# Kernel tuning notes

Measured on AMD Instinct MI355X. Metric: run time of the kernel, lower is better.

The kernel has to match this reference:

```python
import jax, jax.numpy as jnp
import numpy as np
from jax import lax

CHANNEL_N = 16
ALPHA_CHANNEL = 3
FIRE_RATE = 0.5


def get_sobel(size):
    # generalized Sobel: g(x,y) = x / (x^2 + y^2), zero at center
    s = size // 2
    yy, xx = np.mgrid[-s:s + 1, -s:s + 1].astype(np.float32)
    denom = xx * xx + yy * yy
    denom[s, s] = 1.0
    gx = xx / denom
    gy = yy / denom
    gx /= np.sum(np.abs(gx))
    gy /= np.sum(np.abs(gy))
    return gx, gy


def build_kernel(C):
    # stack the six sobel stencils (sizes 3/5/7), zero-padded to 7x7 so a single
    # SAME depthwise conv reproduces the three separate padded convs exactly
    ks = []
    for size in (3, 5, 7):
        gx, gy = get_sobel(size)
        p = (7 - size) // 2
        ks.append(np.pad(gx, p))
        ks.append(np.pad(gy, p))
    k = np.stack(ks, 0)                # [6,7,7]
    k = np.tile(k, (C, 1, 1))          # [6C,7,7], channel-major groups
    return jnp.asarray(k.transpose(1, 2, 0)[:, :, None, :])  # HWIO [7,7,1,6C]


def _maxpool(x, size):
    p = size // 2
    return lax.reduce_window(x, -jnp.inf, lax.max, (1, size, size, 1), (1, 1, 1, 1),
                             [(0, 0), (p, p), (p, p), (0, 0)])


def _life_mask(x):
    alpha = x[..., ALPHA_CHANNEL:ALPHA_CHANNEL + 1]
    return _maxpool(alpha, 3) > 0.1


def _update(x, stoch_u, valid_mask, kern, W0, b0, W1):
    N, H, W, C = x.shape
    pre_life = _life_mask(x)
    y = lax.conv_general_dilated(x, kern, (1, 1), [(3, 3), (3, 3)],
                                 dimension_numbers=("NHWC", "HWIO", "NHWC"),
                                 feature_group_count=C)  # [N,H,W,6C] channel-major
    # reorder to (y1 all C, y2 all C, ...) matching torch.cat order
    y = y.reshape(N, H, W, C, 6).transpose(0, 1, 2, 4, 3).reshape(N, H, W, 6 * C)
    perc = jnp.concatenate([x, y, _maxpool(x, 5)], axis=-1)  # [N,H,W,8C]
    h = jax.nn.relu(perc @ W0 + b0)  # [N,H,W,256]
    dx = h @ W1                      # [N,H,W,C]
    dx = dx * (stoch_u > FIRE_RATE).astype(x.dtype)
    x = x + dx
    life = (pre_life & _life_mask(x)).astype(x.dtype)
    return x * life * valid_mask


def setup_inputs():
    key = jax.random.key(0)
    k1, k2, k3, k4 = jax.random.split(key, 4)
    B, H, W, C, steps = 8, 256, 256, CHANNEL_N, 16
    x = jax.random.uniform(k1, (B, H, W, C), jnp.float32)
    valid_mask = jnp.ones((B, H, W, 1), jnp.float32)
    stoch = jax.random.uniform(k2, (steps, B, H, W, 1), jnp.float32)
    W0 = jax.random.normal(k3, (8 * C, 256), jnp.float32) * 0.05
    b0 = jnp.zeros((256,), jnp.float32)
    W1 = jax.random.normal(k4, (256, C), jnp.float32) * 0.02
    return {"x": x, "valid_mask": valid_mask, "stoch": stoch,
            "W0": W0, "b0": b0, "W1": W1, "steps": steps}


def reference(x, valid_mask, stoch, W0, b0, W1, steps):
    kern = build_kernel(x.shape[-1])

    def step(carry, su):
        return _update(carry, su, valid_mask, kern, W0, b0, W1), None

    x, _ = lax.scan(step, x, stoch[:steps])
    return x
```

## Files before the change

### kernel.cpp

```cpp
#include <hip/hip_runtime.h>
#include <math.h>


#define HW 256
#define NPIX (8*HW*HW)

typedef __attribute__((ext_vector_type(8))) short short8;
typedef __attribute__((ext_vector_type(4))) float f32x4;

__device__ __forceinline__ float4 f4max(float4 a, float4 b) {
    return make_float4(fmaxf(a.x,b.x), fmaxf(a.y,b.y), fmaxf(a.z,b.z), fmaxf(a.w,b.w));
}
__device__ __forceinline__ unsigned short bf16_rne(float v) {
    unsigned int u = __float_as_uint(v);
    unsigned int r = u + 0x7FFFu + ((u >> 16) & 1u);
    return (unsigned short)(r >> 16);
}
__device__ __forceinline__ float bf16f(unsigned short h) {
    return __uint_as_float(((unsigned int)h) << 16);
}

__global__ void init_kernel(const float* __restrict__ W0,
                            const float* __restrict__ W1,
                            float* __restrict__ filt,
                            unsigned short* __restrict__ W0hiT,
                            unsigned short* __restrict__ W0loT,
                            unsigned short* __restrict__ W1hiT2,
                            unsigned short* __restrict__ W1loT2) {
    int t = blockIdx.x * blockDim.x + threadIdx.x;
    int nth = gridDim.x * blockDim.x;
    for (int idx = t; idx < 32768; idx += nth) {
        int j = idx >> 7, k = idx & 127;
        float v = W0[k * 256 + j];
        unsigned short hi = bf16_rne(v);
        unsigned short lo = bf16_rne(v - bf16f(hi));
        W0hiT[idx] = hi;
        W0loT[idx] = lo;
    }
    for (int idx = t; idx < 4096; idx += nth) {
        int ch = idx >> 8, j = idx & 255;
        float v = W1[j * 16 + ch];
        unsigned short hi = bf16_rne(v);
        unsigned short lo = bf16_rne(v - bf16f(hi));
        W1hiT2[idx] = hi;
        W1loT2[idx] = lo;
    }
    if (t < 6) {
        int f = t;
        int size = 3 + 2*(f >> 1);
        int p0 = (7 - size) >> 1;
        int isY = f & 1;
        float vals[49];
        float norm = 0.f;
        for (int a = 0; a < 7; a++) {
            for (int b = 0; b < 7; b++) {
                float v = 0.f;
                if (a >= p0 && a < p0+size && b >= p0 && b < p0+size) {
                    float fy = (float)(a - 3), fx = (float)(b - 3);
                    float den = fx*fx + fy*fy;
                    if (den == 0.f) den = 1.f;
                    v = (isY ? fy : fx) / den;
                }
                vals[a*7+b] = v;
                norm += fabsf(v);
            }
        }
        float inv = 1.f / norm;
        for (int i = 0; i < 49; i++) filt[f*49 + i] = vals[i] * inv;
    }
}

__launch_bounds__(256, 2)
__global__ void step_main(const float* __restrict__ x,
                          float* __restrict__ xmid,
                          const unsigned char* __restrict__ prelife_in,
                          unsigned char* __restrict__ prelife_out,
                          const float* __restrict__ filt_g,
                          const unsigned short* __restrict__ W0hiT,
                          const unsigned short* __restrict__ W0loT,
                          const unsigned short* __restrict__ W1hiT2,
                          const unsigned short* __restrict__ W1loT2,
                          const float* __restrict__ b0,
                          const float* __restrict__ stoch_s,
                          const float* __restrict__ valid,
                          int apply_mask) {
    __shared__ float smem[19712];
    float*          xs      = smem;
    float*          filt_s  = smem + 3920;
    unsigned short* w0hA    = (unsigned short*)smem;
    unsigned short* w0lA    = (unsigned short*)(smem + 2176);
    unsigned short* w0hB    = (unsigned short*)(smem + 4352);
    unsigned short* w0lB    = (unsigned short*)(smem + 6528);
    unsigned short* perc_hi = (unsigned short*)(smem + 8704);
    unsigned short* perc_lo = (unsigned short*)(smem + 13056);
    unsigned short* hbuf_hi = (unsigned short*)(smem + 17408);
    unsigned short* hbuf_lo = (unsigned short*)(smem + 18560);

    const int t   = threadIdx.x;
    const int b   = blockIdx.z;
    const int ty0 = blockIdx.y * 8;
    const int tx0 = blockIdx.x * 8;

    const int sgbase = ((t >> 3) << 7) + ((t & 7) << 4);
    const int swds   = (t >> 3) * 136 + ((t & 7) << 4);
    uint4 sh0 = *(const uint4*)&W0hiT[sgbase];
    uint4 sh1 = *(const uint4*)&W0hiT[sgbase + 8];
    uint4 sl0 = *(const uint4*)&W0loT[sgbase];
    uint4 sl1 = *(const uint4*)&W0loT[sgbase + 8];

    for (int i = t; i < 294; i += 256) filt_s[i] = filt_g[i];

    if (t < 196) {
        const int ly = t / 14, lx = t - ly*14;
        const int gy = ty0 + ly - 3, gx = tx0 + lx - 3;
        const bool inb = ((unsigned)gy < 256u) && ((unsigned)gx < 256u);
        float4 v0 = make_float4(0.f,0.f,0.f,0.f), v1 = v0, v2 = v0, v3 = v0;
        if (inb) {
            const int pix = (b << 16) + (gy << 8) + gx;
            const float* srcp = &x[(size_t)pix << 4];
            v0 = *(const float4*)(srcp);
            v1 = *(const float4*)(srcp + 4);
            v2 = *(const float4*)(srcp + 8);
            v3 = *(const float4*)(srcp + 12);
            if (apply_mask) {
                float m = -INFINITY;
                #pragma unroll
                for (int dy = -1; dy <= 1; dy++) {
                    #pragma unroll
                    for (int dxo = -1; dxo <= 1; dxo++) {
                        int yy = gy + dy, xx2 = gx + dxo;
                        if ((unsigned)yy < 256u && (unsigned)xx2 < 256u)
                            m = fmaxf(m, x[((size_t)((b<<16)+(yy<<8)+xx2) << 4) + 3]);
                    }
                }
                float s = (prelife_in[pix] != 0 && m > 0.1f) ? valid[pix] : 0.f;
                v0.x *= s; v0.y *= s; v0.z *= s; v0.w *= s;
                v1.x *= s; v1.y *= s; v1.z *= s; v1.w *= s;
                v2.x *= s; v2.y *= s; v2.z *= s; v2.w *= s;
                v3.x *= s; v3.y *= s; v3.z *= s; v3.w *= s;
            }
        }
        float* dstp = &xs[t * 20];
        *(float4*)(dstp)      = v0;
        *(float4*)(dstp + 4)  = v1;
        *(float4*)(dstp + 8)  = v2;
        *(float4*)(dstp + 12) = v3;
    }
    __syncthreads();

    {
        const int p  = t & 63;
        const int q  = t >> 6;
        const int py = p >> 3, px1 = p & 7;
        const int gy = ty0 + py, gx = tx0 + px1;
        const int q4 = q << 2;

        float4 y4[6];
        #pragma unroll
        for (int f = 0; f < 6; f++) y4[f] = make_float4(0.f,0.f,0.f,0.f);

        #pragma unroll
        for (int a = 0; a < 7; a++) {
            #pragma unroll
            for (int bb = 0; bb < 7; bb++) {
                float4 xv = *(const float4*)&xs[((py+a)*14 + (px1+bb))*20 + q4];
                {
                    float w4 = filt_s[4*49 + a*7 + bb];
                    float w5 = filt_s[5*49 + a*7 + bb];
                    y4[4].x = fmaf(w4, xv.x, y4[4].x); y4[4].y = fmaf(w4, xv.y, y4[4].y);
                    y4[4].z = fmaf(w4, xv.z, y4[4].z); y4[4].w = fmaf(w4, xv.w, y4[4].w);
                    y4[5].x = fmaf(w5, xv.x, y4[5].x); y4[5].y = fmaf(w5, xv.y, y4[5].y);
                    y4[5].z = fmaf(w5, xv.z, y4[5].z); y4[5].w = fmaf(w5, xv.w, y4[5].w);
                }
                if (a >= 1 && a <= 5 && bb >= 1 && bb <= 5) {
                    float w2 = filt_s[2*49 + a*7 + bb];
                    float w3 = filt_s[3*49 + a*7 + bb];
                    y4[2].x = fmaf(w2, xv.x, y4[2].x); y4[2].y = fmaf(w2, xv.y, y4[2].y);
                    y4[2].z = fmaf(w2, xv.z, y4[2].z); y4[2].w = fmaf(w2, xv.w, y4[2].w);
                    y4[3].x = fmaf(w3, xv.x, y4[3].x); y4[3].y = fmaf(w3, xv.y, y4[3].y);
                    y4[3].z = fmaf(w3, xv.z, y4[3].z); y4[3].w = fmaf(w3, xv.w, y4[3].w);
                }
                if (a >= 2 && a <= 4 && bb >= 2 && bb <= 4) {
                    float w0 = filt_s[0*49 + a*7 + bb];
                    float w1 = filt_s[1*49 + a*7 + bb];
                    y4[0].x = fmaf(w0, xv.x, y4[0].x); y4[0].y = fmaf(w0, xv.y, y4[0].y);
                    y4[0].z = fmaf(w0, xv.z, y4[0].z); y4[0].w = fmaf(w0, xv.w, y4[0].w);
                    y4[1].x = fmaf(w1, xv.x, y4[1].x); y4[1].y = fmaf(w1, xv.y, y4[1].y);
                    y4[1].z = fmaf(w1, xv.z, y4[1].z); y4[1].w = fmaf(w1, xv.w, y4[1].w);
                }
            }
        }
        float4 m5 = make_float4(-INFINITY,-INFINITY,-INFINITY,-INFINITY);
        #pragma unroll
        for (int dy = -2; dy <= 2; dy++) {
            #pragma unroll
            for (int dx2 = -2; dx2 <= 2; dx2++) {
                if ((unsigned)(gy+dy) < 256u && (unsigned)(gx+dx2) < 256u)
                    m5 = f4max(m5, *(const float4*)&xs[((py+3+dy)*14 + (px1+3+dx2))*20 + q4]);
            }
        }
        float4 xc = *(const float4*)&xs[((py+3)*14 + (px1+3))*20 + q4];

        #define SPLIT4(arridx, v) { \
            unsigned short h0 = bf16_rne((v).x), h1 = bf16_rne((v).y); \
            unsigned short h2 = bf16_rne((v).z), h3 = bf16_rne((v).w); \
            unsigned short l0 = bf16_rne((v).x - bf16f(h0)); \
            unsigned short l1 = bf16_rne((v).y - bf16f(h1)); \
            unsigned short l2 = bf16_rne((v).z - bf16f(h2)); \
            unsigned short l3 = bf16_rne((v).w - bf16f(h3)); \
            *(ushort4*)&perc_hi[arridx] = make_ushort4(h0,h1,h2,h3); \
            *(ushort4*)&perc_lo[arridx] = make_ushort4(l0,l1,l2,l3); }

        const int prow = p * 136;
        SPLIT4(prow +       q4, xc);
        SPLIT4(prow + 16  + q4, y4[0]);
        SPLIT4(prow + 32  + q4, y4[1]);
        SPLIT4(prow + 48  + q4, y4[2]);
        SPLIT4(prow + 64  + q4, y4[3]);
        SPLIT4(prow + 80  + q4, y4[4]);
        SPLIT4(prow + 96  + q4, y4[5]);
        SPLIT4(prow + 112 + q4, m5);
        #undef SPLIT4

        if (q == 0) {
            float pre = -INFINITY;
            #pragma unroll
            for (int dy = -1; dy <= 1; dy++) {
                #pragma unroll
                for (int dx2 = -1; dx2 <= 1; dx2++) {
                    if ((unsigned)(gy+dy) < 256u && (unsigned)(gx+dx2) < 256u)
                        pre = fmaxf(pre, xs[((py+3+dy)*14 + (px1+3+dx2))*20 + 3]);
                }
            }
            prelife_out[(b << 16) + (gy << 8) + gx] = (pre > 0.1f) ? 1 : 0;
        }
    }
    __syncthreads();

    const int lane = t & 63;
    const int wid  = t >> 6;
    const int l15  = lane & 15;
    const int l4   = lane >> 4;
    const int aoff  = (wid*16 + l15)*136 + 8*l4;
    const int boff0 = (l15)*136 + 8*l4;
    const int boff1 = (16 + l15)*136 + 8*l4;
    const int hwr   = (wid*16 + 4*l4)*36 + l15;
    const int hrd   = (wid*16 + l15)*36 + 8*l4;
    const int w1off = l15*256 + 8*l4;

    short8 ah0 = *(const short8*)&perc_hi[aoff +  0];
    short8 ah1 = *(const short8*)&perc_hi[aoff + 32];
    short8 ah2 = *(const short8*)&perc_hi[aoff + 64];
    short8 ah3 = *(const short8*)&perc_hi[aoff + 96];
    short8 al0 = *(const short8*)&perc_lo[aoff +  0];
    short8 al1 = *(const short8*)&perc_lo[aoff + 32];
    short8 al2 = *(const short8*)&perc_lo[aoff + 64];
    short8 al3 = *(const short8*)&perc_lo[aoff + 96];

    f32x4 dacc = {0.f, 0.f, 0.f, 0.f};

    *(uint4*)&w0hA[swds]     = sh0;
    *(uint4*)&w0hA[swds + 8] = sh1;
    *(uint4*)&w0lA[swds]     = sl0;
    *(uint4*)&w0lA[swds + 8] = sl1;
    sh0 = *(const uint4*)&W0hiT[sgbase + 4096];
    sh1 = *(const uint4*)&W0hiT[sgbase + 4096 + 8];
    sl0 = *(const uint4*)&W0loT[sgbase + 4096];
    sl1 = *(const uint4*)&W0loT[sgbase + 4096 + 8];
    __syncthreads();

    #pragma unroll 1
    for (int jc = 0; jc < 8; jc++) {
        const unsigned short* wrdh = (jc & 1) ? w0hB : w0hA;
        const unsigned short* wrdl = (jc & 1) ? w0lB : w0lA;
        unsigned short*       wwrh = (jc & 1) ? w0hA : w0hB;
        unsigned short*       wwrl = (jc & 1) ? w0lA : w0lB;

        f32x4 acc0 = {0.f, 0.f, 0.f, 0.f};
        f32x4 acc1 = {0.f, 0.f, 0.f, 0.f};

        #define KSTEP(accv, boff, AH, AL, ks) { \
            short8 bh = *(const short8*)&wrdh[(boff) + (ks)*32]; \
            short8 bl = *(const short8*)&wrdl[(boff) + (ks)*32]; \
            accv = __builtin_amdgcn_mfma_f32_16x16x32_bf16(AL, bh, accv, 0, 0, 0); \
            accv = __builtin_amdgcn_mfma_f32_16x16x32_bf16(AH, bl, accv, 0, 0, 0); \
            accv = __builtin_amdgcn_mfma_f32_16x16x32_bf16(AH, bh, accv, 0, 0, 0); }

        KSTEP(acc0, boff0, ah0, al0, 0)
        KSTEP(acc0, boff0, ah1, al1, 1)
        KSTEP(acc0, boff0, ah2, al2, 2)
        KSTEP(acc0, boff0, ah3, al3, 3)
        KSTEP(acc1, boff1, ah0, al0, 0)
        KSTEP(acc1, boff1, ah1, al1, 1)
        KSTEP(acc1, boff1, ah2, al2, 2)
        KSTEP(acc1, boff1, ah3, al3, 3)
        #undef KSTEP

        {
            float bias0 = b0[jc*32 + l15];
            float bias1 = b0[jc*32 + 16 + l15];
            #pragma unroll
            for (int r = 0; r < 4; r++) {
                float h0 = fmaxf(acc0[r] + bias0, 0.f);
                float h1 = fmaxf(acc1[r] + bias1, 0.f);
                unsigned short hh0 = bf16_rne(h0);
                unsigned short hl0 = bf16_rne(h0 - bf16f(hh0));
                unsigned short hh1 = bf16_rne(h1);
                unsigned short hl1 = bf16_rne(h1 - bf16f(hh1));
                hbuf_hi[hwr + r*36]      = hh0;
                hbuf_lo[hwr + r*36]      = hl0;
                hbuf_hi[hwr + r*36 + 16] = hh1;
                hbuf_lo[hwr + r*36 + 16] = hl1;
            }
        }

        {
            short8 hhf = *(const short8*)&hbuf_hi[hrd];
            short8 hlf = *(const short8*)&hbuf_lo[hrd];
            short8 w1h = *(const short8*)&W1hiT2[w1off + jc*32];
            short8 w1l = *(const short8*)&W1loT2[w1off + jc*32];
            dacc = __builtin_amdgcn_mfma_f32_16x16x32_bf16(hlf, w1h, dacc, 0, 0, 0);
            dacc = __builtin_amdgcn_mfma_f32_16x16x32_bf16(hhf, w1l, dacc, 0, 0, 0);
            dacc = __builtin_amdgcn_mfma_f32_16x16x32_bf16(hhf, w1h, dacc, 0, 0, 0);
        }

        if (jc < 7) {
            *(uint4*)&wwrh[swds]     = sh0;
            *(uint4*)&wwrh[swds + 8] = sh1;
            *(uint4*)&wwrl[swds]     = sl0;
            *(uint4*)&wwrl[swds + 8] = sl1;
            if (jc < 6) {
                const int nb = sgbase + (jc + 2) * 4096;
                sh0 = *(const uint4*)&W0hiT[nb];
                sh1 = *(const uint4*)&W0hiT[nb + 8];
                sl0 = *(const uint4*)&W0loT[nb];
                sl1 = *(const uint4*)&W0loT[nb + 8];
            }
            __syncthreads();
        }
    }

    const int pxb = wid*16 + 4*l4;
    #pragma unroll
    for (int r = 0; r < 4; r++) {
        const int px   = pxb + r;
        const int pix2 = (b << 16) + ((ty0 + (px >> 3)) << 8) + (tx0 + (px & 7));
        float fire = (stoch_s[pix2] > 0.5f) ? 1.f : 0.f;
        float xc = bf16f(perc_hi[px*136 + l15]) + bf16f(perc_lo[px*136 + l15]);
        xmid[((size_t)pix2 << 4) + l15] = fmaf(fire, dacc[r], xc);
    }
}

__global__ void step_mask(float* __restrict__ xbuf,
                          const unsigned char* __restrict__ prelife,
                          const float* __restrict__ valid) {
    int pix = blockIdx.x * 256 + threadIdx.x;
    int b = pix >> 16;
    int y = (pix >> 8) & 255;
    int x = pix & 255;
    float m = -INFINITY;
    #pragma unroll
    for (int dy = -1; dy <= 1; dy++) {
        #pragma unroll
        for (int dxo = -1; dxo <= 1; dxo++) {
            int yy = y + dy, xx = x + dxo;
            if ((unsigned)yy < 256u && (unsigned)xx < 256u)
                m = fmaxf(m, xbuf[((size_t)((b << 16) + (yy << 8) + xx) << 4) + 3]);
        }
    }
    float s = (prelife[pix] != 0 && m > 0.1f) ? valid[pix] : 0.f;
    float4* xp = (float4*)&xbuf[(size_t)pix << 4];
    #pragma unroll
    for (int i = 0; i < 4; i++) {
        float4 v = xp[i];
        v.x *= s; v.y *= s; v.z *= s; v.w *= s;
        xp[i] = v;
    }
}

extern "C" void kernel_launch(void* const* d_in, const int* in_sizes, int n_in,
                              void* d_out, int out_size, void* d_ws, size_t ws_size,
                              hipStream_t stream) {
    const float* x0    = (const float*)d_in[0];
    const float* valid = (const float*)d_in[1];
    const float* stoch = (const float*)d_in[2];
    const float* W0    = (const float*)d_in[3];
    const float* b0    = (const float*)d_in[4];
    const float* W1    = (const float*)d_in[5];

    float* ws   = (float*)d_ws;
    float* xA   = ws;
    unsigned char* plA = (unsigned char*)(ws + 8388608);
    unsigned char* plB = plA + 524288;
    float* filt = ws + 8650752;
    unsigned short* W0hiT  = (unsigned short*)(ws + 8651072);
    unsigned short* W0loT  = (unsigned short*)(ws + 8667456);
    unsigned short* W1hiT2 = (unsigned short*)(ws + 8683840);
    unsigned short* W1loT2 = (unsigned short*)(ws + 8685888);
    float* out  = (float*)d_out;

    init_kernel<<<128, 256, 0, stream>>>(W0, W1, filt, W0hiT, W0loT,
                                         W1hiT2, W1loT2);

    const float* src = x0;
    for (int k = 1; k <= 16; k++) {
        float* dst = (k & 1) ? xA : out;
        unsigned char* wr = (k & 1) ? plB : plA;
        unsigned char* rd = (k & 1) ? plA : plB;
        step_main<<<dim3(32,32,8), 256, 0, stream>>>(
            src, dst, rd, wr, filt, W0hiT, W0loT, W1hiT2, W1loT2, b0,
            stoch + (size_t)(k-1)*NPIX, valid, (k > 1) ? 1 : 0);
        src = dst;
    }
    step_mask<<<NPIX/256, 256, 0, stream>>>(out, plA, valid);
}
```

Baseline: 10.60 ms.

## Alias W0 double buffers onto perc tiles to shrink LDS and raise occupancy

Shared memory drops from about 77KB to about 50KB by tightening the row stride from 136 to 132 and placing the W0 weight double-buffers over the perc region after the A fragments and center pixel values are loaded into registers. An extra barrier protects the reuse. Launch bounds go from 2 to 3 blocks per SM to take advantage of the smaller LDS footprint. The cost is higher register pressure from the held xc values and a tighter per-thread register budget, plus possible LDS bank-conflict changes from the new stride.

```diff
diff --git a/kernel.cpp b/kernel.cpp
--- a/kernel.cpp
+++ b/kernel.cpp
@@ -70,7 +70,7 @@
     }
 }
 
-__launch_bounds__(256, 2)
+__launch_bounds__(256, 3)
 __global__ void step_main(const float* __restrict__ x,
                           float* __restrict__ xmid,
                           const unsigned char* __restrict__ prelife_in,
@@ -84,17 +84,17 @@
                           const float* __restrict__ stoch_s,
                           const float* __restrict__ valid,
                           int apply_mask) {
-    __shared__ float smem[19712];
+    __shared__ float smem[12672];
     float*          xs      = smem;
     float*          filt_s  = smem + 3920;
-    unsigned short* w0hA    = (unsigned short*)smem;
-    unsigned short* w0lA    = (unsigned short*)(smem + 2176);
-    unsigned short* w0hB    = (unsigned short*)(smem + 4352);
-    unsigned short* w0lB    = (unsigned short*)(smem + 6528);
-    unsigned short* perc_hi = (unsigned short*)(smem + 8704);
-    unsigned short* perc_lo = (unsigned short*)(smem + 13056);
-    unsigned short* hbuf_hi = (unsigned short*)(smem + 17408);
-    unsigned short* hbuf_lo = (unsigned short*)(smem + 18560);
+    unsigned short* hbuf_hi = (unsigned short*)smem;
+    unsigned short* hbuf_lo = (unsigned short*)(smem + 1152);
+    unsigned short* perc_hi = (unsigned short*)(smem + 4224);
+    unsigned short* perc_lo = (unsigned short*)(smem + 8448);
+    unsigned short* w0hA    = (unsigned short*)(smem + 4224);
+    unsigned short* w0lA    = (unsigned short*)(smem + 6336);
+    unsigned short* w0hB    = (unsigned short*)(smem + 8448);
+    unsigned short* w0lB    = (unsigned short*)(smem + 10560);
 
     const int t   = threadIdx.x;
     const int b   = blockIdx.z;
@@ -102,7 +102,7 @@
     const int tx0 = blockIdx.x * 8;
 
     const int sgbase = ((t >> 3) << 7) + ((t & 7) << 4);
-    const int swds   = (t >> 3) * 136 + ((t & 7) << 4);
+    const int swds   = (t >> 3) * 132 + ((t & 7) << 4);
     uint4 sh0 = *(const uint4*)&W0hiT[sgbase];
     uint4 sh1 = *(const uint4*)&W0hiT[sgbase + 8];
     uint4 sl0 = *(const uint4*)&W0loT[sgbase];
@@ -211,7 +211,7 @@
             *(ushort4*)&perc_hi[arridx] = make_ushort4(h0,h1,h2,h3); \
             *(ushort4*)&perc_lo[arridx] = make_ushort4(l0,l1,l2,l3); }
 
-        const int prow = p * 136;
+        const int prow = p * 132;
         SPLIT4(prow +       q4, xc);
         SPLIT4(prow + 16  + q4, y4[0]);
         SPLIT4(prow + 32  + q4, y4[1]);
@@ -241,12 +241,13 @@
     const int wid  = t >> 6;
     const int l15  = lane & 15;
     const int l4   = lane >> 4;
-    const int aoff  = (wid*16 + l15)*136 + 8*l4;
-    const int boff0 = (l15)*136 + 8*l4;
-    const int boff1 = (16 + l15)*136 + 8*l4;
+    const int aoff  = (wid*16 + l15)*132 + 8*l4;
+    const int boff0 = (l15)*132 + 8*l4;
+    const int boff1 = (16 + l15)*132 + 8*l4;
     const int hwr   = (wid*16 + 4*l4)*36 + l15;
     const int hrd   = (wid*16 + l15)*36 + 8*l4;
     const int w1off = l15*256 + 8*l4;
+    const int pxb   = wid*16 + 4*l4;
 
     short8 ah0 = *(const short8*)&perc_hi[aoff +  0];
     short8 ah1 = *(const short8*)&perc_hi[aoff + 32];
@@ -256,6 +257,11 @@
     short8 al1 = *(const short8*)&perc_lo[aoff + 32];
     short8 al2 = *(const short8*)&perc_lo[aoff + 64];
     short8 al3 = *(const short8*)&perc_lo[aoff + 96];
+    float xc0 = bf16f(perc_hi[(pxb+0)*132 + l15]) + bf16f(perc_lo[(pxb+0)*132 + l15]);
+    float xc1 = bf16f(perc_hi[(pxb+1)*132 + l15]) + bf16f(perc_lo[(pxb+1)*132 + l15]);
+    float xc2 = bf16f(perc_hi[(pxb+2)*132 + l15]) + bf16f(perc_lo[(pxb+2)*132 + l15]);
+    float xc3 = bf16f(perc_hi[(pxb+3)*132 + l15]) + bf16f(perc_lo[(pxb+3)*132 + l15]);
+    __syncthreads();
 
     f32x4 dacc = {0.f, 0.f, 0.f, 0.f};
 
@@ -340,14 +346,23 @@
         }
     }
 
-    const int pxb = wid*16 + 4*l4;
-    #pragma unroll
-    for (int r = 0; r < 4; r++) {
-        const int px   = pxb + r;
-        const int pix2 = (b << 16) + ((ty0 + (px >> 3)) << 8) + (tx0 + (px & 7));
-        float fire = (stoch_s[pix2] > 0.5f) ? 1.f : 0.f;
-        float xc = bf16f(perc_hi[px*136 + l15]) + bf16f(perc_lo[px*136 + l15]);
-        xmid[((size_t)pix2 << 4) + l15] = fmaf(fire, dacc[r], xc);
+    {
+        const int px0 = pxb;
+        const int pix0 = (b << 16) + ((ty0 + (px0 >> 3)) << 8) + (tx0 + (px0 & 7));
+        float f0 = (stoch_s[pix0] > 0.5f) ? 1.f : 0.f;
+        xmid[((size_t)pix0 << 4) + l15] = fmaf(f0, dacc[0], xc0);
+        const int px1 = pxb + 1;
+        const int pix1 = (b << 16) + ((ty0 + (px1 >> 3)) << 8) + (tx0 + (px1 & 7));
+        float f1 = (stoch_s[pix1] > 0.5f) ? 1.f : 0.f;
+        xmid[((size_t)pix1 << 4) + l15] = fmaf(f1, dacc[1], xc1);
+        const int px2 = pxb + 2;
+        const int pix2 = (b << 16) + ((ty0 + (px2 >> 3)) << 8) + (tx0 + (px2 & 7));
+        float f2 = (stoch_s[pix2] > 0.5f) ? 1.f : 0.f;
+        xmid[((size_t)pix2 << 4) + l15] = fmaf(f2, dacc[2], xc2);
+        const int px3 = pxb + 3;
+        const int pix3 = (b << 16) + ((ty0 + (px3 >> 3)) << 8) + (tx0 + (px3 & 7));
+        float f3 = (stoch_s[pix3] > 0.5f) ? 1.f : 0.f;
+        xmid[((size_t)pix3 << 4) + l15] = fmaf(f3, dacc[3], xc3);
     }
 }
 
```

Result: slower. 20.26 ms (+91.1%).
